# Performance work log

Measured on AMD Instinct MI355X. Metric: run time of the kernel, lower is better.

Reference implementation:

```python
import jax, jax.numpy as jnp
import numpy as np

N_HEAD = 16
N_EMBD = 1024

def setup_inputs() -> dict:
    key = jax.random.key(0)
    ks = jax.random.split(key, 9)
    B, T, C = 4, 2048, N_EMBD
    s = 1.0 / np.sqrt(C)
    return {
        "x": jax.random.normal(ks[0], (B, T, C), dtype=jnp.float32),
        "Wk": jax.random.normal(ks[1], (C, C), dtype=jnp.float32) * s,
        "bk": jnp.zeros((C,), dtype=jnp.float32),
        "Wq": jax.random.normal(ks[2], (C, C), dtype=jnp.float32) * s,
        "bq": jnp.zeros((C,), dtype=jnp.float32),
        "Wv": jax.random.normal(ks[3], (C, C), dtype=jnp.float32) * s,
        "bv": jnp.zeros((C,), dtype=jnp.float32),
        "Wp": jax.random.normal(ks[4], (C, C), dtype=jnp.float32) * s,
        "bp": jnp.zeros((C,), dtype=jnp.float32),
    }

def reference(x, Wk, bk, Wq, bq, Wv, bv, Wp, bp):
    B, T, C = x.shape
    H = N_HEAD
    D = C // H  # head dim
    # linear projections (torch nn.Linear: x @ W^T + b)
    def proj(W, b):
        y = jnp.einsum('btc,oc->bto', x, W) + b
        return y.reshape(B, T, H, D).transpose(0, 2, 1, 3)  # b h t d
    k = proj(Wk, bk)
    q = proj(Wq, bq)
    v = proj(Wv, bv)
    scale = 1.0 / jnp.sqrt(jnp.float32(D))
    att = jnp.einsum('bhtd,bhsd->bhts', q, k) * scale  # [B,H,T,T]
    mask = jnp.tril(jnp.ones((T, T), dtype=bool))
    att = jnp.where(mask[None, None], att, -jnp.inf)
    att = jax.nn.softmax(att, axis=-1)
    y = jnp.einsum('bhts,bhsd->bhtd', att, v)
    y = y.transpose(0, 2, 1, 3).reshape(B, T, C)
    y = jnp.einsum('btc,oc->bto', y, Wp) + bp
    return y
```

## Files before the change

### kernel.cpp

```cpp
#include <hip/hip_runtime.h>
#include <hip/hip_bf16.h>
#include <stdint.h>

#define NH 16
#define CD 1024
#define DD 64
#define TT 2048
#define BB 4
#define MR (BB*TT)

typedef float f32x4 __attribute__((ext_vector_type(4)));
typedef short s16x8 __attribute__((ext_vector_type(8)));

static __device__ __forceinline__ uint16_t f2bf(float f) {
  uint32_t u = __float_as_uint(f);
  u += 0x7FFFu + ((u >> 16) & 1u);
  return (uint16_t)(u >> 16);
}

__global__ __launch_bounds__(256)
void cvt5(const float* __restrict__ x, const float* __restrict__ wq,
          const float* __restrict__ wk, const float* __restrict__ wv,
          const float* __restrict__ wp,
          uint16_t* __restrict__ xb, uint16_t* __restrict__ wqb,
          uint16_t* __restrict__ wkb, uint16_t* __restrict__ wvb,
          uint16_t* __restrict__ wpb)
{
  const int XN8 = (MR*CD)/8;
  const int WN8 = (CD*CD)/8;
  int i = blockIdx.x*256 + threadIdx.x;
  const float* src; uint16_t* dst; int off;
  if (i < XN8) { src = x; dst = xb; off = i; }
  else {
    int r = i - XN8; int ws = r / WN8; off = r - ws*WN8;
    src = (ws==0)?wq:(ws==1)?wk:(ws==2)?wv:wp;
    dst = (ws==0)?wqb:(ws==1)?wkb:(ws==2)?wvb:wpb;
  }
  f32x4 a = *(const f32x4*)&src[(size_t)off*8];
  f32x4 b = *(const f32x4*)&src[(size_t)off*8 + 4];
  s16x8 o;
  o[0]=(short)f2bf(a.x); o[1]=(short)f2bf(a.y); o[2]=(short)f2bf(a.z); o[3]=(short)f2bf(a.w);
  o[4]=(short)f2bf(b.x); o[5]=(short)f2bf(b.y); o[6]=(short)f2bf(b.z); o[7]=(short)f2bf(b.w);
  *(s16x8*)&dst[(size_t)off*8] = o;
}

#define GQ_SBAR  { __builtin_amdgcn_s_barrier(); __builtin_amdgcn_sched_barrier(0); }
#define GQ_LGKM  { asm volatile("s_waitcnt lgkmcnt(0)" ::: "memory"); __builtin_amdgcn_sched_barrier(0); }
#define GQ_VM3   { asm volatile("s_waitcnt vmcnt(3)" ::: "memory"); __builtin_amdgcn_sched_barrier(0); }
#define GQ_VM6   { asm volatile("s_waitcnt vmcnt(6)" ::: "memory"); __builtin_amdgcn_sched_barrier(0); }
#define GQ_VM0   { asm volatile("s_waitcnt vmcnt(0)" ::: "memory"); __builtin_amdgcn_sched_barrier(0); }

__global__ __launch_bounds__(512)
void gemm_qkv8m(const uint16_t* __restrict__ xb, const uint16_t* __restrict__ wqkv,
                const float* __restrict__ bq, const float* __restrict__ bk,
                const float* __restrict__ bv,
                uint16_t* __restrict__ qo, uint16_t* __restrict__ ko,
                uint16_t* __restrict__ vo)
{
  __shared__ __align__(16) uint16_t lA[3][2][128*32];
  __shared__ __align__(16) uint16_t lB[3][2][256*32];

  const int tid = threadIdx.x, lane = tid & 63;
  const int g = lane >> 4, r16 = lane & 15;
  const int w = tid >> 6;
  const int wr = w >> 2, wc = w & 3;
  const int sw8 = ((g ^ ((r16 >> 1) & 3)) << 3);

  const int bid = blockIdx.x;
  const int lin = (bid & 7)*96 + (bid >> 3);
  const int cx = lin >> 6, my = lin & 63;
  const int rowBase = my * 128, colBase = cx * 256;
  const int z = colBase >> 10;
  const bool vt = (z == 2);
  const float* bias  = (z==0) ? bq : (z==1) ? bk : bv;
  uint16_t* Out      = (z==0) ? qo : (z==1) ? ko : vo;
  const float oscale = (z==0) ? 0.125f : 1.0f;

  auto stageA = [&](int buf, int kh, int kt) {
    const int row = w*16 + (lane >> 2);
    const int k = kt*64 + kh*32 + (((lane & 3) ^ ((row >> 1) & 3)) << 3);
    __builtin_amdgcn_global_load_lds(
      (const void*)(xb + (size_t)(rowBase + row)*CD + k),
      (void*)&lA[buf][kh][(w*16)*32], 16, 0, 0);
  };
  auto stageB = [&](int buf, int kh, int kt) {
    #pragma unroll
    for (int c = 0; c < 2; ++c) {
      const int r0 = (c*8 + w)*16;
      const int row = r0 + (lane >> 2);
      const int k = kt*64 + kh*32 + (((lane & 3) ^ ((row >> 1) & 3)) << 3);
      __builtin_amdgcn_global_load_lds(
        (const void*)(wqkv + (size_t)(colBase + row)*CD + k),
        (void*)&lB[buf][kh][r0*32], 16, 0, 0);
    }
  };
  auto stageTile = [&](int buf, int kt) {
    stageA(buf, 0, kt); stageB(buf, 0, kt);
    stageA(buf, 1, kt); stageB(buf, 1, kt);
  };

  f32x4 acc[4][4];
  #pragma unroll
  for (int i = 0; i < 4; ++i)
    #pragma unroll
    for (int j = 0; j < 4; ++j) acc[i][j] = (f32x4){0.f,0.f,0.f,0.f};

  stageTile(0, 0);
  stageTile(1, 1);
  GQ_VM6

  int cur = 0;
  for (int t = 0; t < 16; ++t) {
    const int nxt2 = (cur + 2 >= 3) ? cur - 1 : cur + 2;
    GQ_SBAR
    s16x8 af[2][4], bf[2][4];
    #pragma unroll
    for (int kh = 0; kh < 2; ++kh) {
      #pragma unroll
      for (int i = 0; i < 4; ++i) {
        int row = wr*64 + i*16 + r16;
        af[kh][i] = *(const s16x8*)&lA[cur][kh][row*32 + sw8];
      }
      #pragma unroll
      for (int j = 0; j < 4; ++j) {
        int row = wc*64 + j*16 + r16;
        bf[kh][j] = *(const s16x8*)&lB[cur][kh][row*32 + sw8];
      }
    }
    if (t < 14) stageTile(nxt2, t + 2);
    GQ_LGKM
    __builtin_amdgcn_s_setprio(1);
    if (!vt) {
      #pragma unroll
      for (int kh = 0; kh < 2; ++kh)
        #pragma unroll
        for (int i = 0; i < 4; ++i)
          #pragma unroll
          for (int j = 0; j < 4; ++j)
            acc[i][j] = __builtin_amdgcn_mfma_f32_16x16x32_bf16(af[kh][i], bf[kh][j], acc[i][j], 0,0,0);
    } else {
      #pragma unroll
      for (int kh = 0; kh < 2; ++kh)
        #pragma unroll
        for (int i = 0; i < 4; ++i)
          #pragma unroll
          for (int j = 0; j < 4; ++j)
            acc[i][j] = __builtin_amdgcn_mfma_f32_16x16x32_bf16(bf[kh][j], af[kh][i], acc[i][j], 0,0,0);
    }
    __builtin_amdgcn_s_setprio(0);
    if (t < 14)      GQ_VM6
    else if (t == 14) GQ_VM0
    cur = (cur == 2) ? 0 : cur + 1;
  }

  if (!vt) {
    #pragma unroll
    for (int i = 0; i < 4; ++i)
      #pragma unroll
      for (int j = 0; j < 4; ++j) {
        int n = colBase + wc*64 + j*16 + r16;
        int nl = n & 1023;
        float bb = bias[nl];
        int hh = nl >> 6, d = nl & (DD-1);
        #pragma unroll
        for (int rg = 0; rg < 4; ++rg) {
          int m = rowBase + wr*64 + i*16 + g*4 + rg;
          int b = m >> 11, t2 = m & (TT-1);
          Out[(((size_t)(b*NH + hh))*TT + t2)*DD + d] = f2bf((acc[i][j][rg] + bb) * oscale);
        }
      }
  } else {
    #pragma unroll
    for (int i = 0; i < 4; ++i)
      #pragma unroll
      for (int j = 0; j < 4; ++j) {
        int m = rowBase + wr*64 + i*16 + r16;
        int b = m >> 11, t2 = m & (TT-1);
        #pragma unroll
        for (int rg = 0; rg < 4; ++rg) {
          int n = colBase + wc*64 + j*16 + g*4 + rg;
          int nl = n & 1023;
          float bb = bias[nl];
          int hh = nl >> 6, d = nl & (DD-1);
          Out[(((size_t)(b*NH + hh))*DD + d)*TT + t2] = f2bf(acc[i][j][rg] + bb);
        }
      }
  }
}

#define GP_PHASE(DB, KH, STG, VM) { \
  GQ_SBAR \
  s16x8 af[4], bf[4]; \
  _Pragma("unroll") \
  for (int i = 0; i < 4; ++i) { \
    int row = wr*64 + i*16 + r16; \
    af[i] = *(const s16x8*)&lA[DB][KH][row*32 + sw8]; \
  } \
  _Pragma("unroll") \
  for (int j = 0; j < 4; ++j) { \
    int row = wc*64 + j*16 + r16; \
    bf[j] = *(const s16x8*)&lB[DB][KH][row*32 + sw8]; \
  } \
  STG; \
  GQ_LGKM \
  __builtin_amdgcn_s_setprio(1); \
  _Pragma("unroll") \
  for (int i = 0; i < 4; ++i) \
    _Pragma("unroll") \
    for (int j = 0; j < 4; ++j) \
      acc[i][j] = __builtin_amdgcn_mfma_f32_16x16x32_bf16(af[i], bf[j], acc[i][j], 0,0,0); \
  __builtin_amdgcn_s_setprio(0); \
  VM \
}

__global__ __launch_bounds__(512)
void gemm_proj8(const uint16_t* __restrict__ yb, const uint16_t* __restrict__ wpb,
                const float* __restrict__ bias, float* __restrict__ Out)
{
  __shared__ __align__(16) uint16_t lA[2][2][128*32];
  __shared__ __align__(16) uint16_t lB[2][2][256*32];

  const int tid = threadIdx.x, lane = tid & 63;
  const int g = lane >> 4, r16 = lane & 15;
  const int w = tid >> 6;
  const int wr = w >> 2, wc = w & 3;
  const int sw8 = ((g ^ ((r16 >> 1) & 3)) << 3);

  const int bid = blockIdx.x;
  const int lin = (bid & 7)*32 + (bid >> 3);
  const int cx = lin >> 6, my = lin & 63;
  const int rowBase = my * 128, colBase = cx * 256;

  auto stageA = [&](int dbuf, int kh, int kt) {
    const int row = w*16 + (lane >> 2);
    const int k = kt*64 + kh*32 + (((lane & 3) ^ ((row >> 1) & 3)) << 3);
    __builtin_amdgcn_global_load_lds(
      (const void*)(yb + (size_t)(rowBase + row)*CD + k),
      (void*)&lA[dbuf][kh][(w*16)*32], 16, 0, 0);
  };
  auto stageB = [&](int dbuf, int kh, int kt) {
    #pragma unroll
    for (int c = 0; c < 2; ++c) {
      const int r0 = (c*8 + w)*16;
      const int row = r0 + (lane >> 2);
      const int k = kt*64 + kh*32 + (((lane & 3) ^ ((row >> 1) & 3)) << 3);
      __builtin_amdgcn_global_load_lds(
        (const void*)(wpb + (size_t)(colBase + row)*CD + k),
        (void*)&lB[dbuf][kh][r0*32], 16, 0, 0);
    }
  };

  f32x4 acc[4][4];
  #pragma unroll
  for (int i = 0; i < 4; ++i)
    #pragma unroll
    for (int j = 0; j < 4; ++j) acc[i][j] = (f32x4){0.f,0.f,0.f,0.f};

  stageA(0, 0, 0); stageB(0, 0, 0);
  stageA(0, 1, 0); stageB(0, 1, 0);
  GQ_VM3

  for (int t = 0; t < 8; ++t) {
    const int kt1 = 2*t + 1, kt2 = 2*t + 2;
    const bool last = (t == 7);
    GP_PHASE(0, 0, { stageA(1,0,kt1); stageB(1,0,kt1); }, GQ_VM3)
    GP_PHASE(0, 1, { stageA(1,1,kt1); stageB(1,1,kt1); }, GQ_VM3)
    GP_PHASE(1, 0, if (!last) { stageA(0,0,kt2); stageB(0,0,kt2); },
                   if (!last) GQ_VM3 else GQ_VM0)
    GP_PHASE(1, 1, if (!last) { stageA(0,1,kt2); stageB(0,1,kt2); },
                   if (!last) GQ_VM3)
  }

  #pragma unroll
  for (int i = 0; i < 4; ++i)
    #pragma unroll
    for (int j = 0; j < 4; ++j) {
      int n = colBase + wc*64 + j*16 + r16;
      float bb = bias[n];
      #pragma unroll
      for (int rg = 0; rg < 4; ++rg) {
        int m = rowBase + wr*64 + i*16 + g*4 + rg;
        Out[(size_t)m*CD + n] = acc[i][j][rg] + bb;
      }
    }
}

__global__ __launch_bounds__(256)
void attn128s(const uint16_t* __restrict__ qg, const uint16_t* __restrict__ kg,
              const uint16_t* __restrict__ vtg, uint16_t* __restrict__ yg)
{
  __shared__ __align__(16) uint16_t lK[2][64*64];
  __shared__ __align__(16) uint16_t lV[2][64*64];
  __shared__ __align__(16) uint16_t lP[4][16*64];

  const int tid = threadIdx.x, lane = tid & 63;
  const int g = lane >> 4, r16 = lane & 15;
  const int w = tid >> 6;
  const int id  = blockIdx.x;
  const int xcd = id & 7, idx = id >> 3;
  const int gid = xcd + 8*(idx >> 3);
  const int xq  = idx & 7;
  const int h = gid & 15, b = gid >> 4;
  const size_t kbase = ((size_t)(b*NH + h)) * TT * DD;
  const size_t vbase = ((size_t)(b*NH + h)) * DD * TT;

  const short oe = (r16 == 0) ? (short)0x3F80 : (short)0;
  const s16x8 onesf = {oe,oe,oe,oe,oe,oe,oe,oe};

  auto stage = [&](int cur, int jt) {
    #pragma unroll
    for (int c = 0; c < 2; ++c) {
      int row = w*16 + c*8 + (lane >> 3);
      int sc  = (lane & 7) ^ (row & 7);
      __builtin_amdgcn_global_load_lds(
        (const void*)(kg + kbase + (size_t)(jt*64 + row)*DD + sc*8),
        (void*)&lK[cur][(w*16 + c*8)*64], 16, 0, 0);
      __builtin_amdgcn_global_load_lds(
        (const void*)(vtg + vbase + (size_t)row*TT + jt*64 + sc*8),
        (void*)&lV[cur][(w*16 + c*8)*64], 16, 0, 0);
    }
  };

  for (int ph = 0; ph < 2; ++ph) {
    const int qbi = ph ? 15 - xq : xq;
    const int qrow0 = qbi*128 + w*32;

    s16x8 qf[2][2];
    #pragma unroll
    for (int rb = 0; rb < 2; ++rb)
      #pragma unroll
      for (int ks = 0; ks < 2; ++ks)
        qf[rb][ks] = *(const s16x8*)&qg[kbase + (size_t)(qrow0 + rb*16 + r16)*DD + ks*32 + g*8];

    f32x4 accY[2][4];
    f32x4 accL[2];
    #pragma unroll
    for (int rb = 0; rb < 2; ++rb) {
      #pragma unroll
      for (int i = 0; i < 4; ++i) accY[rb][i] = (f32x4){0.f,0.f,0.f,0.f};
      accL[rb] = (f32x4){0.f,0.f,0.f,0.f};
    }

    const int njt = 2*qbi + 2;
    __syncthreads();
    stage(0, 0);
    int cur = 0;
    for (int jt = 0; jt < njt; ++jt) {
      __syncthreads();
      if (jt + 1 < njt) stage(cur ^ 1, jt + 1);
      if (jt*64 <= qrow0 + 31) {
        f32x4 sacc[2][4];
        #pragma unroll
        for (int rb = 0; rb < 2; ++rb)
          #pragma unroll
          for (int sb = 0; sb < 4; ++sb) sacc[rb][sb] = (f32x4){0.f,0.f,0.f,0.f};
        __builtin_amdgcn_s_setprio(1);
        #pragma unroll
        for (int sb = 0; sb < 4; ++sb)
          #pragma unroll
          for (int ks = 0; ks < 2; ++ks) {
            int row = sb*16 + r16;
            int ch = (ks*4 + g) ^ (row & 7);
            s16x8 kf = *(const s16x8*)&lK[cur][row*64 + ch*8];
            sacc[0][sb] = __builtin_amdgcn_mfma_f32_16x16x32_bf16(qf[0][ks], kf, sacc[0][sb], 0,0,0);
            sacc[1][sb] = __builtin_amdgcn_mfma_f32_16x16x32_bf16(qf[1][ks], kf, sacc[1][sb], 0,0,0);
          }
        __builtin_amdgcn_s_setprio(0);
        s16x8 vfr[2][4];
        #pragma unroll
        for (int ks = 0; ks < 2; ++ks)
          #pragma unroll
          for (int dblk = 0; dblk < 4; ++dblk) {
            int row = dblk*16 + r16;
            int ch = (ks*4 + g) ^ (row & 7);
            vfr[ks][dblk] = *(const s16x8*)&lV[cur][row*64 + ch*8];
          }
        #pragma unroll
        for (int rb = 0; rb < 2; ++rb) {
          const int qr0b = qrow0 + rb*16;
          if (jt*64 > qr0b + 15) continue;
          if (jt*64 + 63 > qr0b) {
            #pragma unroll
            for (int sb = 0; sb < 4; ++sb)
              #pragma unroll
              for (int rg = 0; rg < 4; ++rg)
                if (jt*64 + sb*16 + r16 > qr0b + g*4 + rg) sacc[rb][sb][rg] = -1.0e30f;
          }
          #pragma unroll
          for (int sb = 0; sb < 4; ++sb) {
            int c = sb*16 + r16;
            #pragma unroll
            for (int rgp = 0; rgp < 2; ++rgp) {
              float2 fp;
              fp.x = __expf(sacc[rb][sb][2*rgp]);
              fp.y = __expf(sacc[rb][sb][2*rgp + 1]);
              __hip_bfloat162 h2 = __float22bfloat162_rn(fp);
              uint32_t u = *(uint32_t*)&h2;
              int row0 = g*4 + 2*rgp;
              lP[w][row0*64 + (((c>>3) ^ (row0&7))<<3) + (c&7)] = (uint16_t)(u & 0xffffu);
              int row1 = row0 + 1;
              lP[w][row1*64 + (((c>>3) ^ (row1&7))<<3) + (c&7)] = (uint16_t)(u >> 16);
            }
          }
          s16x8 pf[2];
          #pragma unroll
          for (int ks = 0; ks < 2; ++ks)
            pf[ks] = *(const s16x8*)&lP[w][r16*64 + (((ks*4 + g) ^ (r16&7))<<3)];
          __builtin_amdgcn_s_setprio(1);
          #pragma unroll
          for (int ks = 0; ks < 2; ++ks) {
            #pragma unroll
            for (int dblk = 0; dblk < 4; ++dblk)
              accY[rb][dblk] = __builtin_amdgcn_mfma_f32_16x16x32_bf16(pf[ks], vfr[ks][dblk], accY[rb][dblk], 0,0,0);
            accL[rb] = __builtin_amdgcn_mfma_f32_16x16x32_bf16(pf[ks], onesf, accL[rb], 0,0,0);
          }
          __builtin_amdgcn_s_setprio(0);
        }
      }
      cur ^= 1;
    }

    #pragma unroll
    for (int rb = 0; rb < 2; ++rb) {
      float ls[4];
      #pragma unroll
      for (int rg = 0; rg < 4; ++rg)
        ls[rg] = __shfl(accL[rb][rg], lane & 48);
      #pragma unroll
      for (int dblk = 0; dblk < 4; ++dblk) {
        int d = dblk*16 + r16;
        #pragma unroll
        for (int rg = 0; rg < 4; ++rg) {
          int t = qrow0 + rb*16 + g*4 + rg;
          yg[((size_t)b*TT + t)*CD + h*DD + d] = f2bf(accY[rb][dblk][rg] / ls[rg]);
        }
      }
    }
  }
}

template<int OM>
__global__ __launch_bounds__(256)
void gemm128o(const void* __restrict__ Aptr, const float* __restrict__ W,
              const float* __restrict__ bias, void* __restrict__ Out, float oscale)
{
  __shared__ __align__(16) uint16_t lA[128*40];
  __shared__ __align__(16) uint16_t lB[128*40];
  const int tid = threadIdx.x, lane = tid & 63;
  const int g = lane >> 4, r16 = lane & 15;
  const int w = tid >> 6, wr = w >> 1, wc = w & 1;
  const int rowBase = blockIdx.y * 128, colBase = blockIdx.x * 128;

  f32x4 acc[4][4];
  #pragma unroll
  for (int i = 0; i < 4; ++i)
    #pragma unroll
    for (int j = 0; j < 4; ++j) acc[i][j] = (f32x4){0.f,0.f,0.f,0.f};

  for (int k0 = 0; k0 < CD; k0 += 32) {
    if (OM != 1) {
      const float* A = (const float*)Aptr;
      #pragma unroll
      for (int p = 0; p < 4; ++p) {
        int rr = p*32 + (tid >> 3), kc = (tid & 7)*4;
        f32x4 v = *(const f32x4*)&A[(size_t)(rowBase + rr)*CD + k0 + kc];
        uint64_t pk = (uint64_t)f2bf(v.x) | ((uint64_t)f2bf(v.y)<<16)
                    | ((uint64_t)f2bf(v.z)<<32) | ((uint64_t)f2bf(v.w)<<48);
        *(uint64_t*)&lA[rr*40 + kc] = pk;
      }
    } else {
      const uint16_t* A = (const uint16_t*)Aptr;
      #pragma unroll
      for (int p = 0; p < 2; ++p) {
        int rr = p*64 + (tid >> 2), kc = (tid & 3)*8;
        *(s16x8*)&lA[rr*40 + kc] = *(const s16x8*)&A[(size_t)(rowBase + rr)*CD + k0 + kc];
      }
    }
    #pragma unroll
    for (int p = 0; p < 4; ++p) {
      int rr = p*32 + (tid >> 3), kc = (tid & 7)*4;
      f32x4 v = *(const f32x4*)&W[(size_t)(colBase + rr)*CD + k0 + kc];
      uint64_t pk = (uint64_t)f2bf(v.x) | ((uint64_t)f2bf(v.y)<<16)
                  | ((uint64_t)f2bf(v.z)<<32) | ((uint64_t)f2bf(v.w)<<48);
      *(uint64_t*)&lB[rr*40 + kc] = pk;
    }
    __syncthreads();
    s16x8 af[4], bfr[4];
    #pragma unroll
    for (int i = 0; i < 4; ++i) {
      af[i]  = *(const s16x8*)&lA[(wr*64 + i*16 + r16)*40 + g*8];
      bfr[i] = *(const s16x8*)&lB[(wc*64 + i*16 + r16)*40 + g*8];
    }
    if (OM != 2) {
      #pragma unroll
      for (int i = 0; i < 4; ++i)
        #pragma unroll
        for (int j = 0; j < 4; ++j)
          acc[i][j] = __builtin_amdgcn_mfma_f32_16x16x32_bf16(af[i], bfr[j], acc[i][j], 0,0,0);
    } else {
      #pragma unroll
      for (int i = 0; i < 4; ++i)
        #pragma unroll
        for (int j = 0; j < 4; ++j)
          acc[i][j] = __builtin_amdgcn_mfma_f32_16x16x32_bf16(bfr[j], af[i], acc[i][j], 0,0,0);
    }
    __syncthreads();
  }

  #pragma unroll
  for (int i = 0; i < 4; ++i)
    #pragma unroll
    for (int j = 0; j < 4; ++j) {
      if (OM == 0) {
        int n = colBase + wc*64 + j*16 + r16;
        float bb = bias[n];
        int hh = n >> 6, d = n & (DD-1);
        #pragma unroll
        for (int rg = 0; rg < 4; ++rg) {
          int m = rowBase + wr*64 + i*16 + g*4 + rg;
          int b = m >> 11, t = m & (TT-1);
          ((uint16_t*)Out)[(((size_t)(b*NH + hh))*TT + t)*DD + d] = f2bf((acc[i][j][rg] + bb) * oscale);
        }
      } else if (OM == 1) {
        int n = colBase + wc*64 + j*16 + r16;
        float bb = bias[n];
        #pragma unroll
        for (int rg = 0; rg < 4; ++rg) {
          int m = rowBase + wr*64 + i*16 + g*4 + rg;
          ((float*)Out)[(size_t)m*CD + n] = acc[i][j][rg] + bb;
        }
      } else {
        int m = rowBase + wr*64 + i*16 + r16;
        int b = m >> 11, t = m & (TT-1);
        #pragma unroll
        for (int rg = 0; rg < 4; ++rg) {
          int n = colBase + wc*64 + j*16 + g*4 + rg;
          float bb = bias[n];
          int hh = n >> 6, d = n & (DD-1);
          ((uint16_t*)Out)[(((size_t)(b*NH + hh))*DD + d)*TT + t] = f2bf(acc[i][j][rg] + bb);
        }
      }
    }
}

extern "C" void kernel_launch(void* const* d_in, const int* in_sizes, int n_in,
                              void* d_out, int out_size, void* d_ws, size_t ws_size,
                              hipStream_t stream)
{
  const float* x  = (const float*)d_in[0];
  const float* Wk = (const float*)d_in[1];
  const float* bk = (const float*)d_in[2];
  const float* Wq = (const float*)d_in[3];
  const float* bq = (const float*)d_in[4];
  const float* Wv = (const float*)d_in[5];
  const float* bv = (const float*)d_in[6];
  const float* Wp = (const float*)d_in[7];
  const float* bp = (const float*)d_in[8];
  float* out = (float*)d_out;

  const size_t elems = (size_t)MR * CD;
  const size_t welems = (size_t)CD * CD;

  if (ws_size >= 76ull*1024*1024) {
    uint16_t* xbf = (uint16_t*)d_ws;
    uint16_t* wqb = xbf + elems;
    uint16_t* wkb = wqb + welems;
    uint16_t* wvb = wkb + welems;
    uint16_t* wpb = wvb + welems;
    uint16_t* q_ws = wpb + welems;
    uint16_t* k_ws = q_ws + elems;
    uint16_t* v_ws = k_ws + elems;
    uint16_t* y_ws = xbf;

    cvt5<<<6144, 256, 0, stream>>>(x, Wq, Wk, Wv, Wp, xbf, wqb, wkb, wvb, wpb);
    gemm_qkv8m<<<768, 512, 0, stream>>>(xbf, wqb, bq, bk, bv, q_ws, k_ws, v_ws);
    attn128s<<<512, 256, 0, stream>>>(q_ws, k_ws, v_ws, y_ws);
    gemm_proj8<<<256, 512, 0, stream>>>(y_ws, wpb, bp, out);
  } else {
    uint16_t* q_ws = (uint16_t*)d_ws;
    uint16_t* k_ws = q_ws + elems;
    uint16_t* v_ws = k_ws + elems;
    uint16_t* y_ws = v_ws + elems;
    dim3 gg(CD/128, MR/128);
    gemm128o<0><<<gg, 256, 0, stream>>>(x, Wq, bq, q_ws, 0.125f);
    gemm128o<0><<<gg, 256, 0, stream>>>(x, Wk, bk, k_ws, 1.0f);
    gemm128o<2><<<gg, 256, 0, stream>>>(x, Wv, bv, v_ws, 1.0f);
    attn128s<<<512, 256, 0, stream>>>(q_ws, k_ws, v_ws, y_ws);
    gemm128o<1><<<gg, 256, 0, stream>>>(y_ws, Wp, bp, out, 1.0f);
  }
}
```

Before: 180.2 us.

## Shrink attention query tile to 64 rows and double the grid

```diff
diff --git a/kernel.cpp b/kernel.cpp
--- a/kernel.cpp
+++ b/kernel.cpp
@@ -286,8 +286,8 @@
 }
 
 __global__ __launch_bounds__(256)
-void attn128s(const uint16_t* __restrict__ qg, const uint16_t* __restrict__ kg,
-              const uint16_t* __restrict__ vtg, uint16_t* __restrict__ yg)
+void attn64p(const uint16_t* __restrict__ qg, const uint16_t* __restrict__ kg,
+             const uint16_t* __restrict__ vtg, uint16_t* __restrict__ yg)
 {
   __shared__ __align__(16) uint16_t lK[2][64*64];
   __shared__ __align__(16) uint16_t lV[2][64*64];
@@ -298,8 +298,8 @@
   const int w = tid >> 6;
   const int id  = blockIdx.x;
   const int xcd = id & 7, idx = id >> 3;
-  const int gid = xcd + 8*(idx >> 3);
-  const int xq  = idx & 7;
+  const int gid = xcd + 8*(idx >> 4);
+  const int xq  = idx & 15;
   const int h = gid & 15, b = gid >> 4;
   const size_t kbase = ((size_t)(b*NH + h)) * TT * DD;
   const size_t vbase = ((size_t)(b*NH + h)) * DD * TT;
@@ -322,118 +322,95 @@
   };
 
   for (int ph = 0; ph < 2; ++ph) {
-    const int qbi = ph ? 15 - xq : xq;
-    const int qrow0 = qbi*128 + w*32;
-
-    s16x8 qf[2][2];
-    #pragma unroll
-    for (int rb = 0; rb < 2; ++rb)
-      #pragma unroll
-      for (int ks = 0; ks < 2; ++ks)
-        qf[rb][ks] = *(const s16x8*)&qg[kbase + (size_t)(qrow0 + rb*16 + r16)*DD + ks*32 + g*8];
-
-    f32x4 accY[2][4];
-    f32x4 accL[2];
-    #pragma unroll
-    for (int rb = 0; rb < 2; ++rb) {
-      #pragma unroll
-      for (int i = 0; i < 4; ++i) accY[rb][i] = (f32x4){0.f,0.f,0.f,0.f};
-      accL[rb] = (f32x4){0.f,0.f,0.f,0.f};
-    }
-
-    const int njt = 2*qbi + 2;
+    const int qbi = ph ? 31 - xq : xq;
+    const int qrow0 = qbi*64 + w*16;
+
+    s16x8 qf[2];
+    #pragma unroll
+    for (int ks = 0; ks < 2; ++ks)
+      qf[ks] = *(const s16x8*)&qg[kbase + (size_t)(qrow0 + r16)*DD + ks*32 + g*8];
+
+    f32x4 accY[4];
+    f32x4 accL;
+    #pragma unroll
+    for (int i = 0; i < 4; ++i) accY[i] = (f32x4){0.f,0.f,0.f,0.f};
+    accL = (f32x4){0.f,0.f,0.f,0.f};
+
+    const int njt = qbi + 1;
     __syncthreads();
     stage(0, 0);
     int cur = 0;
     for (int jt = 0; jt < njt; ++jt) {
       __syncthreads();
       if (jt + 1 < njt) stage(cur ^ 1, jt + 1);
-      if (jt*64 <= qrow0 + 31) {
-        f32x4 sacc[2][4];
-        #pragma unroll
-        for (int rb = 0; rb < 2; ++rb)
-          #pragma unroll
-          for (int sb = 0; sb < 4; ++sb) sacc[rb][sb] = (f32x4){0.f,0.f,0.f,0.f};
-        __builtin_amdgcn_s_setprio(1);
+      f32x4 sacc[4];
+      #pragma unroll
+      for (int sb = 0; sb < 4; ++sb) sacc[sb] = (f32x4){0.f,0.f,0.f,0.f};
+      __builtin_amdgcn_s_setprio(1);
+      #pragma unroll
+      for (int sb = 0; sb < 4; ++sb)
+        #pragma unroll
+        for (int ks = 0; ks < 2; ++ks) {
+          int row = sb*16 + r16;
+          int ch = (ks*4 + g) ^ (row & 7);
+          s16x8 kf = *(const s16x8*)&lK[cur][row*64 + ch*8];
+          sacc[sb] = __builtin_amdgcn_mfma_f32_16x16x32_bf16(qf[ks], kf, sacc[sb], 0,0,0);
+        }
+      __builtin_amdgcn_s_setprio(0);
+      if (jt*64 + 63 > qrow0) {
         #pragma unroll
         for (int sb = 0; sb < 4; ++sb)
           #pragma unroll
-          for (int ks = 0; ks < 2; ++ks) {
-            int row = sb*16 + r16;
-            int ch = (ks*4 + g) ^ (row & 7);
-            s16x8 kf = *(const s16x8*)&lK[cur][row*64 + ch*8];
-            sacc[0][sb] = __builtin_amdgcn_mfma_f32_16x16x32_bf16(qf[0][ks], kf, sacc[0][sb], 0,0,0);
-            sacc[1][sb] = __builtin_amdgcn_mfma_f32_16x16x32_bf16(qf[1][ks], kf, sacc[1][sb], 0,0,0);
-          }
-        __builtin_amdgcn_s_setprio(0);
-        s16x8 vfr[2][4];
-        #pragma unroll
-        for (int ks = 0; ks < 2; ++ks)
-          #pragma unroll
-          for (int dblk = 0; dblk < 4; ++dblk) {
-            int row = dblk*16 + r16;
-            int ch = (ks*4 + g) ^ (row & 7);
-            vfr[ks][dblk] = *(const s16x8*)&lV[cur][row*64 + ch*8];
-          }
-        #pragma unroll
-        for (int rb = 0; rb < 2; ++rb) {
-          const int qr0b = qrow0 + rb*16;
-          if (jt*64 > qr0b + 15) continue;
-          if (jt*64 + 63 > qr0b) {
-            #pragma unroll
-            for (int sb = 0; sb < 4; ++sb)
-              #pragma unroll
-              for (int rg = 0; rg < 4; ++rg)
-                if (jt*64 + sb*16 + r16 > qr0b + g*4 + rg) sacc[rb][sb][rg] = -1.0e30f;
-          }
-          #pragma unroll
-          for (int sb = 0; sb < 4; ++sb) {
-            int c = sb*16 + r16;
-            #pragma unroll
-            for (int rgp = 0; rgp < 2; ++rgp) {
-              float2 fp;
-              fp.x = __expf(sacc[rb][sb][2*rgp]);
-              fp.y = __expf(sacc[rb][sb][2*rgp + 1]);
-              __hip_bfloat162 h2 = __float22bfloat162_rn(fp);
-              uint32_t u = *(uint32_t*)&h2;
-              int row0 = g*4 + 2*rgp;
-              lP[w][row0*64 + (((c>>3) ^ (row0&7))<<3) + (c&7)] = (uint16_t)(u & 0xffffu);
-              int row1 = row0 + 1;
-              lP[w][row1*64 + (((c>>3) ^ (row1&7))<<3) + (c&7)] = (uint16_t)(u >> 16);
-            }
-          }
-          s16x8 pf[2];
-          #pragma unroll
-          for (int ks = 0; ks < 2; ++ks)
-            pf[ks] = *(const s16x8*)&lP[w][r16*64 + (((ks*4 + g) ^ (r16&7))<<3)];
-          __builtin_amdgcn_s_setprio(1);
-          #pragma unroll
-          for (int ks = 0; ks < 2; ++ks) {
-            #pragma unroll
-            for (int dblk = 0; dblk < 4; ++dblk)
-              accY[rb][dblk] = __builtin_amdgcn_mfma_f32_16x16x32_bf16(pf[ks], vfr[ks][dblk], accY[rb][dblk], 0,0,0);
-            accL[rb] = __builtin_amdgcn_mfma_f32_16x16x32_bf16(pf[ks], onesf, accL[rb], 0,0,0);
-          }
-          __builtin_amdgcn_s_setprio(0);
-        }
-      }
+          for (int rg = 0; rg < 4; ++rg)
+            if (jt*64 + sb*16 + r16 > qrow0 + g*4 + rg) sacc[sb][rg] = -1.0e30f;
+      }
+      #pragma unroll
+      for (int sb = 0; sb < 4; ++sb) {
+        int c = sb*16 + r16;
+        #pragma unroll
+        for (int rgp = 0; rgp < 2; ++rgp) {
+          float2 fp;
+          fp.x = __expf(sacc[sb][2*rgp]);
+          fp.y = __expf(sacc[sb][2*rgp + 1]);
+          __hip_bfloat162 h2 = __float22bfloat162_rn(fp);
+          uint32_t u = *(uint32_t*)&h2;
+          int row0 = g*4 + 2*rgp;
+          lP[w][row0*64 + (((c>>3) ^ (row0&7))<<3) + (c&7)] = (uint16_t)(u & 0xffffu);
+          int row1 = row0 + 1;
+          lP[w][row1*64 + (((c>>3) ^ (row1&7))<<3) + (c&7)] = (uint16_t)(u >> 16);
+        }
+      }
+      s16x8 pf[2];
+      #pragma unroll
+      for (int ks = 0; ks < 2; ++ks)
+        pf[ks] = *(const s16x8*)&lP[w][r16*64 + (((ks*4 + g) ^ (r16&7))<<3)];
+      __builtin_amdgcn_s_setprio(1);
+      #pragma unroll
+      for (int ks = 0; ks < 2; ++ks) {
+        #pragma unroll
+        for (int dblk = 0; dblk < 4; ++dblk) {
+          int row = dblk*16 + r16;
+          int ch = (ks*4 + g) ^ (row & 7);
+          s16x8 vf = *(const s16x8*)&lV[cur][row*64 + ch*8];
+          accY[dblk] = __builtin_amdgcn_mfma_f32_16x16x32_bf16(pf[ks], vf, accY[dblk], 0,0,0);
+        }
+        accL = __builtin_amdgcn_mfma_f32_16x16x32_bf16(pf[ks], onesf, accL, 0,0,0);
+      }
+      __builtin_amdgcn_s_setprio(0);
       cur ^= 1;
     }
 
-    #pragma unroll
-    for (int rb = 0; rb < 2; ++rb) {
-      float ls[4];
-      #pragma unroll
-      for (int rg = 0; rg < 4; ++rg)
-        ls[rg] = __shfl(accL[rb][rg], lane & 48);
-      #pragma unroll
-      for (int dblk = 0; dblk < 4; ++dblk) {
-        int d = dblk*16 + r16;
-        #pragma unroll
-        for (int rg = 0; rg < 4; ++rg) {
-          int t = qrow0 + rb*16 + g*4 + rg;
-          yg[((size_t)b*TT + t)*CD + h*DD + d] = f2bf(accY[rb][dblk][rg] / ls[rg]);
-        }
+    float ls[4];
+    #pragma unroll
+    for (int rg = 0; rg < 4; ++rg)
+      ls[rg] = __shfl(accL[rg], lane & 48);
+    #pragma unroll
+    for (int dblk = 0; dblk < 4; ++dblk) {
+      int d = dblk*16 + r16;
+      #pragma unroll
+      for (int rg = 0; rg < 4; ++rg) {
+        int t = qrow0 + g*4 + rg;
+        yg[((size_t)b*TT + t)*CD + h*DD + d] = f2bf(accY[dblk][rg] / ls[rg]);
       }
     }
   }
@@ -574,7 +551,7 @@
 
     cvt5<<<6144, 256, 0, stream>>>(x, Wq, Wk, Wv, Wp, xbf, wqb, wkb, wvb, wpb);
     gemm_qkv8m<<<768, 512, 0, stream>>>(xbf, wqb, bq, bk, bv, q_ws, k_ws, v_ws);
-    attn128s<<<512, 256, 0, stream>>>(q_ws, k_ws, v_ws, y_ws);
+    attn64p<<<1024, 256, 0, stream>>>(q_ws, k_ws, v_ws, y_ws);
     gemm_proj8<<<256, 512, 0, stream>>>(y_ws, wpb, bp, out);
   } else {
     uint16_t* q_ws = (uint16_t*)d_ws;
@@ -585,7 +562,7 @@
     gemm128o<0><<<gg, 256, 0, stream>>>(x, Wq, bq, q_ws, 0.125f);
     gemm128o<0><<<gg, 256, 0, stream>>>(x, Wk, bk, k_ws, 1.0f);
     gemm128o<2><<<gg, 256, 0, stream>>>(x, Wv, bv, v_ws, 1.0f);
-    attn128s<<<512, 256, 0, stream>>>(q_ws, k_ws, v_ws, y_ws);
+    attn64p<<<1024, 256, 0, stream>>>(q_ws, k_ws, v_ws, y_ws);
     gemm128o<1><<<gg, 256, 0, stream>>>(y_ws, Wp, bp, out, 1.0f);
   }
 }
```

Result: slower. 189.4 us (+5.1%).

## Triple-buffer projection GEMM and fold log2e into Q scale for raw exp2

Applied to the files above, without the earlier changes.

```diff
diff --git a/kernel.cpp b/kernel.cpp
--- a/kernel.cpp
+++ b/kernel.cpp
@@ -8,6 +8,8 @@
 #define TT 2048
 #define BB 4
 #define MR (BB*TT)
+
+#define QSCALE (0.125f * 1.44269504f)
 
 typedef float f32x4 __attribute__((ext_vector_type(4)));
 typedef short s16x8 __attribute__((ext_vector_type(8)));
@@ -46,7 +48,6 @@
 
 #define GQ_SBAR  { __builtin_amdgcn_s_barrier(); __builtin_amdgcn_sched_barrier(0); }
 #define GQ_LGKM  { asm volatile("s_waitcnt lgkmcnt(0)" ::: "memory"); __builtin_amdgcn_sched_barrier(0); }
-#define GQ_VM3   { asm volatile("s_waitcnt vmcnt(3)" ::: "memory"); __builtin_amdgcn_sched_barrier(0); }
 #define GQ_VM6   { asm volatile("s_waitcnt vmcnt(6)" ::: "memory"); __builtin_amdgcn_sched_barrier(0); }
 #define GQ_VM0   { asm volatile("s_waitcnt vmcnt(0)" ::: "memory"); __builtin_amdgcn_sched_barrier(0); }
 
@@ -74,7 +75,7 @@
   const bool vt = (z == 2);
   const float* bias  = (z==0) ? bq : (z==1) ? bk : bv;
   uint16_t* Out      = (z==0) ? qo : (z==1) ? ko : vo;
-  const float oscale = (z==0) ? 0.125f : 1.0f;
+  const float oscale = (z==0) ? QSCALE : 1.0f;
 
   auto stageA = [&](int buf, int kh, int kt) {
     const int row = w*16 + (lane >> 2);
@@ -188,37 +189,12 @@
   }
 }
 
-#define GP_PHASE(DB, KH, STG, VM) { \
-  GQ_SBAR \
-  s16x8 af[4], bf[4]; \
-  _Pragma("unroll") \
-  for (int i = 0; i < 4; ++i) { \
-    int row = wr*64 + i*16 + r16; \
-    af[i] = *(const s16x8*)&lA[DB][KH][row*32 + sw8]; \
-  } \
-  _Pragma("unroll") \
-  for (int j = 0; j < 4; ++j) { \
-    int row = wc*64 + j*16 + r16; \
-    bf[j] = *(const s16x8*)&lB[DB][KH][row*32 + sw8]; \
-  } \
-  STG; \
-  GQ_LGKM \
-  __builtin_amdgcn_s_setprio(1); \
-  _Pragma("unroll") \
-  for (int i = 0; i < 4; ++i) \
-    _Pragma("unroll") \
-    for (int j = 0; j < 4; ++j) \
-      acc[i][j] = __builtin_amdgcn_mfma_f32_16x16x32_bf16(af[i], bf[j], acc[i][j], 0,0,0); \
-  __builtin_amdgcn_s_setprio(0); \
-  VM \
-}
-
 __global__ __launch_bounds__(512)
-void gemm_proj8(const uint16_t* __restrict__ yb, const uint16_t* __restrict__ wpb,
-                const float* __restrict__ bias, float* __restrict__ Out)
+void gemm_proj8m(const uint16_t* __restrict__ yb, const uint16_t* __restrict__ wpb,
+                 const float* __restrict__ bias, float* __restrict__ Out)
 {
-  __shared__ __align__(16) uint16_t lA[2][2][128*32];
-  __shared__ __align__(16) uint16_t lB[2][2][256*32];
+  __shared__ __align__(16) uint16_t lA[3][2][128*32];
+  __shared__ __align__(16) uint16_t lB[3][2][256*32];
 
   const int tid = threadIdx.x, lane = tid & 63;
   const int g = lane >> 4, r16 = lane & 15;
@@ -231,14 +207,14 @@
   const int cx = lin >> 6, my = lin & 63;
   const int rowBase = my * 128, colBase = cx * 256;
 
-  auto stageA = [&](int dbuf, int kh, int kt) {
+  auto stageA = [&](int buf, int kh, int kt) {
     const int row = w*16 + (lane >> 2);
     const int k = kt*64 + kh*32 + (((lane & 3) ^ ((row >> 1) & 3)) << 3);
     __builtin_amdgcn_global_load_lds(
       (const void*)(yb + (size_t)(rowBase + row)*CD + k),
-      (void*)&lA[dbuf][kh][(w*16)*32], 16, 0, 0);
-  };
-  auto stageB = [&](int dbuf, int kh, int kt) {
+      (void*)&lA[buf][kh][(w*16)*32], 16, 0, 0);
+  };
+  auto stageB = [&](int buf, int kh, int kt) {
     #pragma unroll
     for (int c = 0; c < 2; ++c) {
       const int r0 = (c*8 + w)*16;
@@ -246,8 +222,12 @@
       const int k = kt*64 + kh*32 + (((lane & 3) ^ ((row >> 1) & 3)) << 3);
       __builtin_amdgcn_global_load_lds(
         (const void*)(wpb + (size_t)(colBase + row)*CD + k),
-        (void*)&lB[dbuf][kh][r0*32], 16, 0, 0);
-    }
+        (void*)&lB[buf][kh][r0*32], 16, 0, 0);
+    }
+  };
+  auto stageTile = [&](int buf, int kt) {
+    stageA(buf, 0, kt); stageB(buf, 0, kt);
+    stageA(buf, 1, kt); stageB(buf, 1, kt);
   };
 
   f32x4 acc[4][4];
@@ -256,19 +236,42 @@
     #pragma unroll
     for (int j = 0; j < 4; ++j) acc[i][j] = (f32x4){0.f,0.f,0.f,0.f};
 
-  stageA(0, 0, 0); stageB(0, 0, 0);
-  stageA(0, 1, 0); stageB(0, 1, 0);
-  GQ_VM3
-
-  for (int t = 0; t < 8; ++t) {
-    const int kt1 = 2*t + 1, kt2 = 2*t + 2;
-    const bool last = (t == 7);
-    GP_PHASE(0, 0, { stageA(1,0,kt1); stageB(1,0,kt1); }, GQ_VM3)
-    GP_PHASE(0, 1, { stageA(1,1,kt1); stageB(1,1,kt1); }, GQ_VM3)
-    GP_PHASE(1, 0, if (!last) { stageA(0,0,kt2); stageB(0,0,kt2); },
-                   if (!last) GQ_VM3 else GQ_VM0)
-    GP_PHASE(1, 1, if (!last) { stageA(0,1,kt2); stageB(0,1,kt2); },
-                   if (!last) GQ_VM3)
+  stageTile(0, 0);
+  stageTile(1, 1);
+  GQ_VM6
+
+  int cur = 0;
+  for (int t = 0; t < 16; ++t) {
+    const int nxt2 = (cur + 2 >= 3) ? cur - 1 : cur + 2;
+    GQ_SBAR
+    s16x8 af[2][4], bf[2][4];
+    #pragma unroll
+    for (int kh = 0; kh < 2; ++kh) {
+      #pragma unroll
+      for (int i = 0; i < 4; ++i) {
+        int row = wr*64 + i*16 + r16;
+        af[kh][i] = *(const s16x8*)&lA[cur][kh][row*32 + sw8];
+      }
+      #pragma unroll
+      for (int j = 0; j < 4; ++j) {
+        int row = wc*64 + j*16 + r16;
+        bf[kh][j] = *(const s16x8*)&lB[cur][kh][row*32 + sw8];
+      }
+    }
+    if (t < 14) stageTile(nxt2, t + 2);
+    GQ_LGKM
+    __builtin_amdgcn_s_setprio(1);
+    #pragma unroll
+    for (int kh = 0; kh < 2; ++kh)
+      #pragma unroll
+      for (int i = 0; i < 4; ++i)
+        #pragma unroll
+        for (int j = 0; j < 4; ++j)
+          acc[i][j] = __builtin_amdgcn_mfma_f32_16x16x32_bf16(af[kh][i], bf[kh][j], acc[i][j], 0,0,0);
+    __builtin_amdgcn_s_setprio(0);
+    if (t < 14)      GQ_VM6
+    else if (t == 14) GQ_VM0
+    cur = (cur == 2) ? 0 : cur + 1;
   }
 
   #pragma unroll
@@ -392,8 +395,8 @@
             #pragma unroll
             for (int rgp = 0; rgp < 2; ++rgp) {
               float2 fp;
-              fp.x = __expf(sacc[rb][sb][2*rgp]);
-              fp.y = __expf(sacc[rb][sb][2*rgp + 1]);
+              asm("v_exp_f32 %0, %1" : "=v"(fp.x) : "v"(sacc[rb][sb][2*rgp]));
+              asm("v_exp_f32 %0, %1" : "=v"(fp.y) : "v"(sacc[rb][sb][2*rgp + 1]));
               __hip_bfloat162 h2 = __float22bfloat162_rn(fp);
               uint32_t u = *(uint32_t*)&h2;
               int row0 = g*4 + 2*rgp;
@@ -575,14 +578,14 @@
     cvt5<<<6144, 256, 0, stream>>>(x, Wq, Wk, Wv, Wp, xbf, wqb, wkb, wvb, wpb);
     gemm_qkv8m<<<768, 512, 0, stream>>>(xbf, wqb, bq, bk, bv, q_ws, k_ws, v_ws);
     attn128s<<<512, 256, 0, stream>>>(q_ws, k_ws, v_ws, y_ws);
-    gemm_proj8<<<256, 512, 0, stream>>>(y_ws, wpb, bp, out);
+    gemm_proj8m<<<256, 512, 0, stream>>>(y_ws, wpb, bp, out);
   } else {
     uint16_t* q_ws = (uint16_t*)d_ws;
     uint16_t* k_ws = q_ws + elems;
     uint16_t* v_ws = k_ws + elems;
     uint16_t* y_ws = v_ws + elems;
     dim3 gg(CD/128, MR/128);
-    gemm128o<0><<<gg, 256, 0, stream>>>(x, Wq, bq, q_ws, 0.125f);
+    gemm128o<0><<<gg, 256, 0, stream>>>(x, Wq, bq, q_ws, QSCALE);
     gemm128o<0><<<gg, 256, 0, stream>>>(x, Wk, bk, k_ws, 1.0f);
     gemm128o<2><<<gg, 256, 0, stream>>>(x, Wv, bv, v_ws, 1.0f);
     attn128s<<<512, 256, 0, stream>>>(q_ws, k_ws, v_ws, y_ws);
```

Result: faster. 170.7 us (median of 2 runs) (-5.2%).
